# Kernel tuning notes

Hardware: AMD Instinct MI355X
Metric: run time of the kernel (lower is better)

Reference implementation:

```python
import jax, jax.numpy as jnp
import numpy as np

DIM = 1024
B = 65536


def setup_inputs() -> dict:
    key = jax.random.key(0)
    k1, k2, k3 = jax.random.split(key, 3)
    x_l = jax.random.normal(k1, (B, DIM), dtype=jnp.float32)
    x_0 = jax.random.normal(k2, (B, DIM), dtype=jnp.float32)
    # xavier_uniform for w of shape (dim, 1): bound = sqrt(6/(dim+1))
    bound = float(np.sqrt(6.0 / (DIM + 1)))
    w = jax.random.uniform(k3, (DIM, 1), dtype=jnp.float32, minval=-bound, maxval=bound)
    b = jnp.zeros((DIM, 1), dtype=jnp.float32)
    return {"x_l": x_l, "x_0": x_0, "w": w, "b": b}


def reference(x_l, x_0, w, b):
    # Original: (x_0 @ x_l^T) @ w + b + x_l  (per-example outer product).
    # By associativity: x_0 * (x_l . w) + b + x_l, avoiding the B x dim x dim intermediate.
    s = x_l @ w                      # [B, 1] == x_l . w per example
    out = x_0 * s + b[:, 0] + x_l    # broadcast bias over batch
    return out
```

## Files before the change

### kernel.cpp

```cpp
#include <hip/hip_runtime.h>


#define DIM 1024
#define BLOCK 256

__global__ __launch_bounds__(BLOCK) void dcn_fused_kernel(
    const float* __restrict__ x_l,
    const float* __restrict__ x_0,
    const float* __restrict__ w,
    const float* __restrict__ b,
    float* __restrict__ out)
{
    const int wave = threadIdx.x >> 6;
    const int lane = threadIdx.x & 63;
    const int row  = blockIdx.x * 4 + wave;
    const size_t rowbase = (size_t)row * DIM;
    const int c0 = lane * 4;

    float4 xl[4], x0[4], wv[4], bv[4];
    #pragma unroll
    for (int k = 0; k < 4; ++k)
        xl[k] = *(const float4*)(x_l + rowbase + k * 256 + c0);
    #pragma unroll
    for (int k = 0; k < 4; ++k)
        x0[k] = *(const float4*)(x_0 + rowbase + k * 256 + c0);
    #pragma unroll
    for (int k = 0; k < 4; ++k)
        wv[k] = *(const float4*)(w + k * 256 + c0);
    #pragma unroll
    for (int k = 0; k < 4; ++k)
        bv[k] = *(const float4*)(b + k * 256 + c0);

    float partial = 0.0f;
    #pragma unroll
    for (int k = 0; k < 4; ++k) {
        partial = fmaf(xl[k].x, wv[k].x, partial);
        partial = fmaf(xl[k].y, wv[k].y, partial);
        partial = fmaf(xl[k].z, wv[k].z, partial);
        partial = fmaf(xl[k].w, wv[k].w, partial);
    }

    #pragma unroll
    for (int off = 1; off < 64; off <<= 1)
        partial += __shfl_xor(partial, off, 64);
    const float s = partial;

    #pragma unroll
    for (int k = 0; k < 4; ++k) {
        float4 o;
        o.x = fmaf(x0[k].x, s, bv[k].x + xl[k].x);
        o.y = fmaf(x0[k].y, s, bv[k].y + xl[k].y);
        o.z = fmaf(x0[k].z, s, bv[k].z + xl[k].z);
        o.w = fmaf(x0[k].w, s, bv[k].w + xl[k].w);
        *(float4*)(out + rowbase + k * 256 + c0) = o;
    }
}

extern "C" void kernel_launch(void* const* d_in, const int* in_sizes, int n_in,
                              void* d_out, int out_size, void* d_ws, size_t ws_size,
                              hipStream_t stream) {
    const float* x_l = (const float*)d_in[0];
    const float* x_0 = (const float*)d_in[1];
    const float* w   = (const float*)d_in[2];
    const float* b   = (const float*)d_in[3];
    float* out = (float*)d_out;

    const int B = in_sizes[0] / DIM;
    dcn_fused_kernel<<<B / 4, BLOCK, 0, stream>>>(x_l, x_0, w, b, out);
}
```

Baseline: 572.6 us.

## Process multiple rows per wave with double-buffered register prefetch

Each wave now handles 16 consecutive rows instead of one. It loads w and b once, then prefetches the next row's x_l and x_0 into a second register set while computing the current row. This amortizes the per-row w and b loads and launch overhead and keeps more loads in flight per wave. In exchange the grid shrinks to far fewer blocks and register pressure rises, which could reduce occupancy and latency hiding.

```diff
diff --git a/kernel.cpp b/kernel.cpp
--- a/kernel.cpp
+++ b/kernel.cpp
@@ -3,56 +3,104 @@
 
 #define DIM 1024
 #define BLOCK 256
+#define WAVES_PER_BLOCK 4
+#define ROWS_PER_WAVE 16
 
-__global__ __launch_bounds__(BLOCK) void dcn_fused_kernel(
+__global__ __launch_bounds__(BLOCK, 4) void dcn_fused_kernel(
     const float* __restrict__ x_l,
     const float* __restrict__ x_0,
     const float* __restrict__ w,
     const float* __restrict__ b,
     float* __restrict__ out)
 {
-    const int wave = threadIdx.x >> 6;
-    const int lane = threadIdx.x & 63;
-    const int row  = blockIdx.x * 4 + wave;
-    const size_t rowbase = (size_t)row * DIM;
-    const int c0 = lane * 4;
+    const int wave  = threadIdx.x >> 6;
+    const int lane  = threadIdx.x & 63;
+    const int gwave = blockIdx.x * WAVES_PER_BLOCK + wave;
+    const int c0    = lane * 4;
 
-    float4 xl[4], x0[4], wv[4], bv[4];
+    float4 wv[4], bv[4];
     #pragma unroll
-    for (int k = 0; k < 4; ++k)
-        xl[k] = *(const float4*)(x_l + rowbase + k * 256 + c0);
+    for (int k = 0; k < 4; ++k) wv[k] = *(const float4*)(w + k * 256 + c0);
     #pragma unroll
-    for (int k = 0; k < 4; ++k)
-        x0[k] = *(const float4*)(x_0 + rowbase + k * 256 + c0);
-    #pragma unroll
-    for (int k = 0; k < 4; ++k)
-        wv[k] = *(const float4*)(w + k * 256 + c0);
-    #pragma unroll
-    for (int k = 0; k < 4; ++k)
-        bv[k] = *(const float4*)(b + k * 256 + c0);
+    for (int k = 0; k < 4; ++k) bv[k] = *(const float4*)(b + k * 256 + c0);
 
-    float partial = 0.0f;
-    #pragma unroll
-    for (int k = 0; k < 4; ++k) {
-        partial = fmaf(xl[k].x, wv[k].x, partial);
-        partial = fmaf(xl[k].y, wv[k].y, partial);
-        partial = fmaf(xl[k].z, wv[k].z, partial);
-        partial = fmaf(xl[k].w, wv[k].w, partial);
-    }
+    const size_t base = (size_t)gwave * ROWS_PER_WAVE * DIM + (size_t)c0;
+    const float* pl = x_l + base;
+    const float* p0 = x_0 + base;
+    float*       po = out + base;
+
+    float4 xlA[4], x0A[4], xlB[4], x0B[4];
 
     #pragma unroll
-    for (int off = 1; off < 64; off <<= 1)
-        partial += __shfl_xor(partial, off, 64);
-    const float s = partial;
+    for (int k = 0; k < 4; ++k) xlA[k] = *(const float4*)(pl + k * 256);
+    #pragma unroll
+    for (int k = 0; k < 4; ++k) x0A[k] = *(const float4*)(p0 + k * 256);
 
     #pragma unroll
-    for (int k = 0; k < 4; ++k) {
-        float4 o;
-        o.x = fmaf(x0[k].x, s, bv[k].x + xl[k].x);
-        o.y = fmaf(x0[k].y, s, bv[k].y + xl[k].y);
-        o.z = fmaf(x0[k].z, s, bv[k].z + xl[k].z);
-        o.w = fmaf(x0[k].w, s, bv[k].w + xl[k].w);
-        *(float4*)(out + rowbase + k * 256 + c0) = o;
+    for (int r = 0; r < ROWS_PER_WAVE; r += 2) {
+        #pragma unroll
+        for (int k = 0; k < 4; ++k) xlB[k] = *(const float4*)(pl + DIM + k * 256);
+        #pragma unroll
+        for (int k = 0; k < 4; ++k) x0B[k] = *(const float4*)(p0 + DIM + k * 256);
+
+        {
+            float partial = 0.0f;
+            #pragma unroll
+            for (int k = 0; k < 4; ++k) {
+                partial = fmaf(xlA[k].x, wv[k].x, partial);
+                partial = fmaf(xlA[k].y, wv[k].y, partial);
+                partial = fmaf(xlA[k].z, wv[k].z, partial);
+                partial = fmaf(xlA[k].w, wv[k].w, partial);
+            }
+            #pragma unroll
+            for (int off = 1; off < 64; off <<= 1)
+                partial += __shfl_xor(partial, off, 64);
+            const float s = partial;
+            #pragma unroll
+            for (int k = 0; k < 4; ++k) {
+                float4 o;
+                o.x = fmaf(x0A[k].x, s, bv[k].x + xlA[k].x);
+                o.y = fmaf(x0A[k].y, s, bv[k].y + xlA[k].y);
+                o.z = fmaf(x0A[k].z, s, bv[k].z + xlA[k].z);
+                o.w = fmaf(x0A[k].w, s, bv[k].w + xlA[k].w);
+                *(float4*)(po + k * 256) = o;
+            }
+        }
+
+        if (r + 2 < ROWS_PER_WAVE) {
+            #pragma unroll
+            for (int k = 0; k < 4; ++k) xlA[k] = *(const float4*)(pl + 2 * DIM + k * 256);
+            #pragma unroll
+            for (int k = 0; k < 4; ++k) x0A[k] = *(const float4*)(p0 + 2 * DIM + k * 256);
+        }
+
+        {
+            float partial = 0.0f;
+            #pragma unroll
+            for (int k = 0; k < 4; ++k) {
+                partial = fmaf(xlB[k].x, wv[k].x, partial);
+                partial = fmaf(xlB[k].y, wv[k].y, partial);
+                partial = fmaf(xlB[k].z, wv[k].z, partial);
+                partial = fmaf(xlB[k].w, wv[k].w, partial);
+            }
+            #pragma unroll
+            for (int off = 1; off < 64; off <<= 1)
+                partial += __shfl_xor(partial, off, 64);
+            const float s = partial;
+            #pragma unroll
+            for (int k = 0; k < 4; ++k) {
+                float4 o;
+                o.x = fmaf(x0B[k].x, s, bv[k].x + xlB[k].x);
+                o.y = fmaf(x0B[k].y, s, bv[k].y + xlB[k].y);
+                o.z = fmaf(x0B[k].z, s, bv[k].z + xlB[k].z);
+                o.w = fmaf(x0B[k].w, s, bv[k].w + xlB[k].w);
+                *(float4*)(po + DIM + k * 256) = o;
+            }
+        }
+
+        pl += 2 * DIM;
+        p0 += 2 * DIM;
+        po += 2 * DIM;
     }
 }
 
@@ -66,5 +114,6 @@
     float* out = (float*)d_out;
 
     const int B = in_sizes[0] / DIM;
-    dcn_fused_kernel<<<B / 4, BLOCK, 0, stream>>>(x_l, x_0, w, b, out);
+    const int grid = B / (WAVES_PER_BLOCK * ROWS_PER_WAVE);
+    dcn_fused_kernel<<<grid, BLOCK, 0, stream>>>(x_l, x_0, w, b, out);
 }
```

Result: slower. 596.9 us (+4.2%).
